# Kernel optimization log

Hardware: AMD Instinct MI355X
Metric: run time of the kernel (lower is better)

## Reference

```python
import math
import jax, jax.numpy as jnp
import numpy as np

D_MODEL = 1024
N_HEADS = 16
BLOCK = 2048
EPS2 = 0.0487        # sparse_eps2 / BOOTSTRAP_EPS2
ROPE_BASE = 10000.0


def _riemann_zeros(K):
    """Approximate imaginary parts of the first K nontrivial zeta zeros by
    Newton-inverting t/(2pi)*log(t/(2pi*e)) = n - 7/8 (standard asymptotic).
    Note: gamma is normalized by gamma[0] in the module, so only the relative
    spacing matters for the math."""
    n = np.arange(1, K + 1, dtype=np.float64)
    t = 10.0 + 6.0 * n  # safe init, > 2*pi
    for _ in range(60):
        f = t / (2 * np.pi) * np.log(t / (2 * np.pi * np.e)) - (n - 0.875)
        fp = np.log(t / (2 * np.pi)) / (2 * np.pi)
        t = t - f / fp
    return t


def _constants(N, K):
    g = _riemann_zeros(K)
    g = g / g[0]
    denom = 0.25 + g * g
    w_re = (0.5 / denom).astype(np.float32)          # [K]
    w_im = (-g / denom).astype(np.float32)           # [K]
    pos = np.arange(N, dtype=np.float32)
    k_idx = np.arange(K, dtype=np.float32)
    inv_freq = ROPE_BASE ** (-k_idx / K)
    phase = pos[:, None] * inv_freq[None, :]          # [N,K]
    cos_p = np.cos(phase).astype(np.float32)
    sin_p = np.sin(phase).astype(np.float32)
    log1p = np.log1p(pos)
    log_decay = (0.5 * (log1p[None, :] - log1p[:, None])).astype(np.float32)  # [N,N]
    tril = np.tril(np.ones((N, N), dtype=bool))
    return (jnp.asarray(w_re), jnp.asarray(w_im), jnp.asarray(cos_p),
            jnp.asarray(sin_p), jnp.asarray(log_decay), jnp.asarray(tril))


def setup_inputs() -> dict:
    key = jax.random.key(0)
    kx, kq, kk, kv, ko = jax.random.split(key, 5)
    B, N, D = 2, BLOCK, D_MODEL
    s = 0.02
    return {
        "x": jax.random.normal(kx, (B, N, D), jnp.float32),
        "Wq": jax.random.normal(kq, (D, D), jnp.float32) * s,
        "Wk": jax.random.normal(kk, (D, D), jnp.float32) * s,
        "Wv": jax.random.normal(kv, (D, D), jnp.float32) * s,
        "Wo": jax.random.normal(ko, (D, D), jnp.float32) * s,
    }


def reference(x, Wq, Wk, Wv, Wo):
    B, N, D = x.shape
    H = N_HEADS
    dh = D // H
    K = dh // 2
    w_re, w_im, cos_p, sin_p, log_decay, tril = _constants(N, K)

    q = (x @ Wq).reshape(B, N, H, dh)
    k = (x @ Wk).reshape(B, N, H, dh)
    v = (x @ Wv).reshape(B, N, H, dh)

    q_re, q_im = q[..., 0::2], q[..., 1::2]           # [B,N,H,K]
    k_re, k_im = k[..., 0::2], k[..., 1::2]

    cos_b = cos_p[None, :, None, :]                   # [1,N,1,K]
    sin_b = sin_p[None, :, None, :]
    # RoPE rotation in complex form
    qt_re = cos_b * q_re + sin_b * q_im
    qt_im = cos_b * q_im - sin_b * q_re
    kt_re = cos_b * k_re + sin_b * k_im
    kt_im = cos_b * k_im - sin_b * k_re

    wr = w_re[None, None, None, :]
    wi = w_im[None, None, None, :]
    # zeta-amplitude complex weighting of q
    qh_re = wr * qt_re - wi * qt_im
    qh_im = wr * qt_im + wi * qt_re

    # Re(sum_k w_k * q~_i conj(k~_j)) via two real GEMMs
    scores = (jnp.einsum('bihk,bjhk->bhij', qh_re, kt_re)
              + jnp.einsum('bihk,bjhk->bhij', qh_im, kt_im)) / math.sqrt(dh)

    # decay_mode == 'mult'
    scores = scores * jnp.exp(log_decay)[None, None, :, :]

    scores = jnp.where(tril[None, None, :, :], scores, -jnp.inf)
    attn = jax.nn.softmax(scores, axis=-1)

    # bootstrap_sparse: keep top-k per row, renormalize
    kk = max(1, math.ceil(EPS2 * N))
    if kk < N:
        vals, _ = jax.lax.top_k(attn, kk)
        thresh = vals[..., -1:]
        mask = (attn >= thresh).astype(attn.dtype)
        masked = attn * mask
        attn = masked / jnp.maximum(masked.sum(-1, keepdims=True), 1e-9)

    out = jnp.einsum('bhij,bjhd->bihd', attn, v).reshape(B, N, D)
    return out @ Wo
```

## Files before the change

### kernel.cpp

```cpp
#include <hip/hip_runtime.h>
#include <math.h>

#define B_SZ 2
#define N_SEQ 2048
#define DM 1024
#define H_HEADS 16
#define DH 64
#define KC 32
#define TOPK 100
#define TQ 16
#define KT 128
#define NTMAX 16
#define FCAP 192

typedef _Float16 half2_t __attribute__((ext_vector_type(2)));
typedef _Float16 half4_t __attribute__((ext_vector_type(4)));
typedef _Float16 half8_t __attribute__((ext_vector_type(8)));
typedef float floatx4 __attribute__((ext_vector_type(4)));
typedef unsigned short ushort4_t __attribute__((ext_vector_type(4)));

__device__ __forceinline__ unsigned short h2us(_Float16 h) {
  unsigned short u; __builtin_memcpy(&u, &h, 2); return u;
}
__device__ __forceinline__ _Float16 us2h(unsigned short u) {
  _Float16 h; __builtin_memcpy(&h, &u, 2); return h;
}
__device__ __forceinline__ unsigned okey16(unsigned short us) {
  return (us & 0x8000u) ? (unsigned)(unsigned short)~us
                        : (unsigned)(us | 0x8000u);
}

__device__ __forceinline__ void stage16(const _Float16* g, _Float16* lds_base,
                                        int lane) {
#if __has_builtin(__builtin_amdgcn_global_load_lds)
  __builtin_amdgcn_global_load_lds(
      (const __attribute__((address_space(1))) void*)g,
      (__attribute__((address_space(3))) void*)lds_base, 16, 0, 0);
#else
  *(half8_t*)(lds_base + lane * 8) = *(const half8_t*)g;
#endif
}

__global__ void const_kernel(float* __restrict__ wre, float* __restrict__ wim) {
  __shared__ double g0s;
  const int k = threadIdx.x;
  const double PI = 3.14159265358979323846;
  const double E_ = 2.71828182845904523536;
  double n = (double)(k + 1);
  double t = 10.0 + 6.0 * n;
  for (int it = 0; it < 60; ++it) {
    double f  = t / (2.0 * PI) * log(t / (2.0 * PI * E_)) - (n - 0.875);
    double fp = log(t / (2.0 * PI)) / (2.0 * PI);
    t = t - f / fp;
  }
  if (k == 0) g0s = t;
  __syncthreads();
  double g = t / g0s;
  double denom = 0.25 + g * g;
  wre[k] = (float)(0.5 / denom);
  wim[k] = (float)(-g / denom);
}

__global__ __launch_bounds__(256) void rope_kernel(float* __restrict__ cosT,
                                                   float* __restrict__ sinT) {
  int idx = blockIdx.x * 256 + threadIdx.x;
  int kk = idx & 31, n = idx >> 5;
  double inv_freq = pow(10000.0, -(double)kk / 32.0);
  double ph = (double)n * inv_freq;
  cosT[idx] = (float)cos(ph);
  sinT[idx] = (float)sin(ph);
}

__global__ __launch_bounds__(256) void cast_x(const float* __restrict__ x,
                                              _Float16* __restrict__ xh) {
  int idx = blockIdx.x * 256 + threadIdx.x;
  float4 v = ((const float4*)x)[idx];
  half4_t h;
  h[0] = (_Float16)v.x; h[1] = (_Float16)v.y;
  h[2] = (_Float16)v.z; h[3] = (_Float16)v.w;
  ((half4_t*)xh)[idx] = h;
}

__global__ __launch_bounds__(256) void transpose_cast(
    const float* __restrict__ W0, const float* __restrict__ W1,
    const float* __restrict__ W2, const float* __restrict__ W3,
    _Float16* __restrict__ T0, _Float16* __restrict__ T1,
    _Float16* __restrict__ T2, _Float16* __restrict__ T3) {
  __shared__ float t[64][65];
  const float* W; _Float16* T;
  switch (blockIdx.z) {
    case 0: W = W0; T = T0; break;
    case 1: W = W1; T = T1; break;
    case 2: W = W2; T = T2; break;
    default: W = W3; T = T3; break;
  }
  const int bx = blockIdx.x;
  const int by = blockIdx.y;
  const int tid = threadIdx.x;
  const int c = tid & 15, rr = tid >> 4;
#pragma unroll
  for (int i = 0; i < 4; ++i) {
    int k = rr + i * 16;
    float4 v = *(const float4*)(W + (size_t)(bx * 64 + k) * DM + by * 64 + c * 4);
    t[k][c * 4 + 0] = v.x; t[k][c * 4 + 1] = v.y;
    t[k][c * 4 + 2] = v.z; t[k][c * 4 + 3] = v.w;
  }
  __syncthreads();
#pragma unroll
  for (int i = 0; i < 4; ++i) {
    int n = rr + i * 16;
    half4_t h;
    h[0] = (_Float16)t[c * 4 + 0][n];
    h[1] = (_Float16)t[c * 4 + 1][n];
    h[2] = (_Float16)t[c * 4 + 2][n];
    h[3] = (_Float16)t[c * 4 + 3][n];
    *(half4_t*)(T + (size_t)(by * 64 + n) * DM + bx * 64 + c * 4) = h;
  }
}

template <typename OutT>
__device__ __forceinline__ void gemm_mfma_body(const _Float16* __restrict__ A,
                                               const _Float16* __restrict__ Bt,
                                               OutT* __restrict__ C) {
  __shared__ _Float16 As[128 * 32];
  __shared__ _Float16 Bs[128 * 32];
  const int tid = threadIdx.x;
  const int wave = tid >> 6, lane = tid & 63;
  const int wm = wave >> 1, wn = wave & 1;
  const int bm = blockIdx.x * 128, bn = blockIdx.y * 128;
  const int lrow = lane >> 2;
  const int lkb = (lane & 3) * 8;
  const int l16 = lane & 15, lq = lane >> 4;
  floatx4 acc[4][4] = {};

  for (int k0 = 0; k0 < DM; k0 += 32) {
    __syncthreads();
#pragma unroll
    for (int s2 = 0; s2 < 2; ++s2) {
      const int seg = wave * 2 + s2;
      stage16(A + (size_t)(bm + seg * 16 + lrow) * DM + k0 + lkb,
              As + seg * 512, lane);
      stage16(Bt + (size_t)(bn + seg * 16 + lrow) * DM + k0 + lkb,
              Bs + seg * 512, lane);
    }
    __syncthreads();
    half8_t af[4], bf[4];
#pragma unroll
    for (int mi = 0; mi < 4; ++mi)
      af[mi] = *(const half8_t*)(As + (wm * 64 + mi * 16 + l16) * 32 + lq * 8);
#pragma unroll
    for (int ni = 0; ni < 4; ++ni)
      bf[ni] = *(const half8_t*)(Bs + (wn * 64 + ni * 16 + l16) * 32 + lq * 8);
#pragma unroll
    for (int mi = 0; mi < 4; ++mi)
#pragma unroll
      for (int ni = 0; ni < 4; ++ni)
        acc[mi][ni] = __builtin_amdgcn_mfma_f32_16x16x32_f16(
            af[mi], bf[ni], acc[mi][ni], 0, 0, 0);
  }
#pragma unroll
  for (int mi = 0; mi < 4; ++mi)
#pragma unroll
    for (int ni = 0; ni < 4; ++ni) {
      const int col = bn + wn * 64 + ni * 16 + l16;
#pragma unroll
      for (int r = 0; r < 4; ++r) {
        const int row = bm + wm * 64 + mi * 16 + lq * 4 + r;
        C[(size_t)row * DM + col] = (OutT)acc[mi][ni][r];
      }
    }
}

__global__ __launch_bounds__(256) void gemm_qkv_mfma(
    const _Float16* __restrict__ xh, const _Float16* __restrict__ Wt0,
    const _Float16* __restrict__ Wt1, const _Float16* __restrict__ Wt2,
    _Float16* __restrict__ q, _Float16* __restrict__ k,
    _Float16* __restrict__ v) {
  const _Float16* Bt; _Float16* C;
  if (blockIdx.z == 0)      { Bt = Wt0; C = q; }
  else if (blockIdx.z == 1) { Bt = Wt1; C = k; }
  else                      { Bt = Wt2; C = v; }
  gemm_mfma_body<_Float16>(xh, Bt, C);
}

__global__ __launch_bounds__(256) void gemm_out_mfma(
    const _Float16* __restrict__ A, const _Float16* __restrict__ Bt,
    float* __restrict__ C) {
  gemm_mfma_body<float>(A, Bt, C);
}

__global__ __launch_bounds__(256) void transform_kernel(
    const _Float16* __restrict__ q, const _Float16* __restrict__ k,
    const _Float16* __restrict__ v, const float* __restrict__ wre,
    const float* __restrict__ wim, const float* __restrict__ cosT,
    const float* __restrict__ sinT, float* __restrict__ qh,
    _Float16* __restrict__ kth, _Float16* __restrict__ vth) {
  int idx = blockIdx.x * blockDim.x + threadIdx.x;
  int kk = idx & 31;
  int h  = (idx >> 5) & 15;
  int n  = (idx >> 9) & 2047;
  int b  = idx >> 20;

  size_t base_in = ((size_t)(b * N_SEQ + n)) * DM + h * DH;
  float q_re = (float)q[base_in + 2 * kk], q_im = (float)q[base_in + 2 * kk + 1];
  float k_re = (float)k[base_in + 2 * kk], k_im = (float)k[base_in + 2 * kk + 1];

  float cp = cosT[n * 32 + kk], sp = sinT[n * 32 + kk];

  float qt_re = cp * q_re + sp * q_im;
  float qt_im = cp * q_im - sp * q_re;
  float ktr   = cp * k_re + sp * k_im;
  float kti   = cp * k_im - sp * k_re;

  float wr = wre[kk], wi = wim[kk];
  float qh_re = wr * qt_re - wi * qt_im;
  float qh_im = wr * qt_im + wi * qt_re;

  float sj = 0.125f * sqrtf(1.0f + (float)n);

  size_t base_out = ((size_t)((b * H_HEADS + h) * N_SEQ + n)) * DH;
  qh[base_out + kk]      = qh_re;
  qh[base_out + 32 + kk] = qh_im;
  kth[base_out + kk]      = (_Float16)(ktr * sj);
  kth[base_out + 32 + kk] = (_Float16)(kti * sj);
  vth[base_out + 2 * kk]     = v[base_in + 2 * kk];
  vth[base_out + 2 * kk + 1] = v[base_in + 2 * kk + 1];
}

__global__ __launch_bounds__(512, 4) void attn_kernel(
    const float* __restrict__ qh, const _Float16* __restrict__ kth,
    const _Float16* __restrict__ vth, _Float16* __restrict__ oh) {
  __shared__ __align__(16) _Float16 ktile[KT][76];
  __shared__ unsigned hist[TQ][128];
  __shared__ unsigned final_[TQ][FCAP];
  __shared__ float mredw[8][TQ];
  __shared__ float rowm[TQ], rowsum[TQ];
  __shared__ unsigned cnt2[TQ], tkA[TQ];
  __shared__ int sh_b[TQ], sh_k[TQ];

  const int tile = gridDim.x - 1 - blockIdx.x;
  const int bh   = blockIdx.y;
  const int i0   = tile * TQ;
  const int tid  = threadIdx.x;
  const int wv = tid >> 6, lane = tid & 63;
  const int l16 = lane & 15, lq = lane >> 4;
  const int jbase = wv * 16 + l16;

  const _Float16* kbase = kth + (size_t)bh * N_SEQ * DH;
  const _Float16* vbase = vth + (size_t)bh * N_SEQ * DH;

#pragma unroll
  for (int u = 0; u < 4; ++u) ((unsigned*)hist)[u * 512 + tid] = 0;
  if (tid < TQ) { cnt2[tid] = 0; rowsum[tid] = 0.f; }

  half8_t af0, af1;
  {
    const float* qrow = qh + ((size_t)(bh * N_SEQ + i0 + l16)) * DH;
    const float rs = rsqrtf(1.0f + (float)(i0 + l16));
    float4 a0 = *(const float4*)(qrow + lq * 8);
    float4 a1 = *(const float4*)(qrow + lq * 8 + 4);
    float4 b0 = *(const float4*)(qrow + 32 + lq * 8);
    float4 b1 = *(const float4*)(qrow + 32 + lq * 8 + 4);
    af0[0] = (_Float16)(a0.x * rs); af0[1] = (_Float16)(a0.y * rs);
    af0[2] = (_Float16)(a0.z * rs); af0[3] = (_Float16)(a0.w * rs);
    af0[4] = (_Float16)(a1.x * rs); af0[5] = (_Float16)(a1.y * rs);
    af0[6] = (_Float16)(a1.z * rs); af0[7] = (_Float16)(a1.w * rs);
    af1[0] = (_Float16)(b0.x * rs); af1[1] = (_Float16)(b0.y * rs);
    af1[2] = (_Float16)(b0.z * rs); af1[3] = (_Float16)(b0.w * rs);
    af1[4] = (_Float16)(b1.x * rs); af1[5] = (_Float16)(b1.y * rs);
    af1[6] = (_Float16)(b1.z * rs); af1[7] = (_Float16)(b1.w * rs);
  }

  const int ntile = (i0 + TQ + KT - 1) / KT;

  ushort4_t scr[NTMAX];
  float mx[4] = {-INFINITY, -INFINITY, -INFINITY, -INFINITY};

#pragma unroll
  for (int t = 0; t < NTMAX; ++t) {
    if (t < ntile) {
      const int j0 = t * KT;
      __syncthreads();
#pragma unroll
      for (int u = 0; u < 2; ++u) {
        int idx = u * 512 + tid;
        int row = idx >> 3, c8 = idx & 7;
        *(half8_t*)&ktile[row][c8 * 8] =
            *(const half8_t*)(kbase + (size_t)(j0 + row) * DH + c8 * 8);
      }
      __syncthreads();
      half8_t bf0 = *(const half8_t*)&ktile[jbase][lq * 8];
      half8_t bf1 = *(const half8_t*)&ktile[jbase][32 + lq * 8];
      floatx4 acc = {};
      acc = __builtin_amdgcn_mfma_f32_16x16x32_f16(af0, bf0, acc, 0, 0, 0);
      acc = __builtin_amdgcn_mfma_f32_16x16x32_f16(af1, bf1, acc, 0, 0, 0);
      const int jc = j0 + jbase;
      ushort4_t s4;
#pragma unroll
      for (int r = 0; r < 4; ++r) {
        float sc = acc[r];
        s4[r] = h2us((_Float16)sc);
        if (jc <= i0 + lq * 4 + r) {
          mx[r] = fmaxf(mx[r], sc);
          unsigned hb = okey16(s4[r]) >> 8;
          atomicAdd(&hist[lq * 4 + r][hb >> 1], 1u << ((hb & 1) * 16));
        }
      }
      scr[t] = s4;
    }
  }

#pragma unroll
  for (int g = 1; g <= 8; g <<= 1)
#pragma unroll
    for (int r = 0; r < 4; ++r) mx[r] = fmaxf(mx[r], __shfl_xor(mx[r], g));
  if (l16 == 0)
#pragma unroll
    for (int r = 0; r < 4; ++r) mredw[wv][lq * 4 + r] = mx[r];
  __syncthreads();
  if (tid < TQ) {
    float m = mredw[0][tid];
#pragma unroll
    for (int w = 1; w < 8; ++w) m = fmaxf(m, mredw[w][tid]);
    rowm[tid] = m;
  }

  const int srow = tid >> 5, ts = tid & 31;
  {
    const int L = i0 + srow + 1;
    if (L > TOPK) {
      const unsigned* hrow = hist[srow];
      const int base_u = 124 - 4 * ts;
      unsigned h0 = hrow[base_u + 0], h1 = hrow[base_u + 1];
      unsigned h2 = hrow[base_u + 2], h3 = hrow[base_u + 3];
      int c[8] = {(int)(h3 >> 16), (int)(h3 & 0xffffu),
                  (int)(h2 >> 16), (int)(h2 & 0xffffu),
                  (int)(h1 >> 16), (int)(h1 & 0xffffu),
                  (int)(h0 >> 16), (int)(h0 & 0xffffu)};
      int ssum = 0;
#pragma unroll
      for (int k2 = 0; k2 < 8; ++k2) ssum += c[k2];
      int inc = ssum;
#pragma unroll
      for (int d = 1; d < 32; d <<= 1) {
        int o = __shfl_up(inc, d, 32);
        if (ts >= d) inc += o;
      }
      const int excl = inc - ssum;
      if (excl < TOPK && TOPK <= inc) {
        int cum = excl, k2 = 0;
#pragma unroll
        for (; k2 < 8; ++k2) {
          if (cum + c[k2] >= TOPK) break;
          cum += c[k2];
        }
        sh_b[srow] = 255 - 8 * ts - k2;
        sh_k[srow] = TOPK - cum;
      }
    } else if (ts == 0) {
      sh_b[srow] = 256;
      sh_k[srow] = 0;
      tkA[srow] = 0;
    }
  }
  __syncthreads();
#pragma unroll
  for (int u = 0; u < 4; ++u) ((unsigned*)hist)[u * 512 + tid] = 0;
  int bh4[4];
#pragma unroll
  for (int r = 0; r < 4; ++r) bh4[r] = sh_b[lq * 4 + r];
  __syncthreads();

#pragma unroll
  for (int t = 0; t < NTMAX; ++t) {
    if (t < ntile) {
      const int jc = t * KT + jbase;
      ushort4_t s4 = scr[t];
#pragma unroll
      for (int r = 0; r < 4; ++r) {
        if (jc <= i0 + lq * 4 + r) {
          unsigned key = okey16(s4[r]);
          if ((int)(key >> 8) == bh4[r]) {
            unsigned lb = key & 255u;
            atomicAdd(&hist[lq * 4 + r][lb >> 1], 1u << ((lb & 1) * 16));
          }
        }
      }
    }
  }
  __syncthreads();

  {
    const int L = i0 + srow + 1;
    if (L > TOPK) {
      const int krem = sh_k[srow];
      const unsigned* hrow = hist[srow];
      const int base_u = 124 - 4 * ts;
      unsigned h0 = hrow[base_u + 0], h1 = hrow[base_u + 1];
      unsigned h2 = hrow[base_u + 2], h3 = hrow[base_u + 3];
      int c[8] = {(int)(h3 >> 16), (int)(h3 & 0xffffu),
                  (int)(h2 >> 16), (int)(h2 & 0xffffu),
                  (int)(h1 >> 16), (int)(h1 & 0xffffu),
                  (int)(h0 >> 16), (int)(h0 & 0xffffu)};
      int ssum = 0;
#pragma unroll
      for (int k2 = 0; k2 < 8; ++k2) ssum += c[k2];
      int inc = ssum;
#pragma unroll
      for (int d = 1; d < 32; d <<= 1) {
        int o = __shfl_up(inc, d, 32);
        if (ts >= d) inc += o;
      }
      const int excl = inc - ssum;
      if (excl < krem && krem <= inc) {
        int cum = excl, k2 = 0;
#pragma unroll
        for (; k2 < 8; ++k2) {
          if (cum + c[k2] >= krem) break;
          cum += c[k2];
        }
        tkA[srow] = ((unsigned)sh_b[srow] << 8) | (unsigned)(255 - 8 * ts - k2);
      }
    }
  }
  __syncthreads();

  unsigned tk4[4]; float m4[4];
#pragma unroll
  for (int r = 0; r < 4; ++r) {
    tk4[r] = tkA[lq * 4 + r];
    m4[r]  = rowm[lq * 4 + r];
  }
  float lsum[4] = {0.f, 0.f, 0.f, 0.f};
#pragma unroll
  for (int t = 0; t < NTMAX; ++t) {
    if (t < ntile) {
      const int jc = t * KT + jbase;
      ushort4_t s4 = scr[t];
#pragma unroll
      for (int r = 0; r < 4; ++r) {
        if (jc <= i0 + lq * 4 + r) {
          unsigned short us = s4[r];
          if (okey16(us) >= tk4[r]) {
            float p = expf((float)us2h(us) - m4[r]);
            lsum[r] += p;
            unsigned pos = atomicAdd(&cnt2[lq * 4 + r], 1u);
            if (pos < FCAP)
              final_[lq * 4 + r][pos] =
                  ((unsigned)h2us((_Float16)p) << 16) | (unsigned)jc;
          }
        }
      }
    }
  }
#pragma unroll
  for (int g = 1; g <= 8; g <<= 1)
#pragma unroll
    for (int r = 0; r < 4; ++r) lsum[r] += __shfl_xor(lsum[r], g);
  if (l16 == 0)
#pragma unroll
    for (int r = 0; r < 4; ++r) atomicAdd(&rowsum[lq * 4 + r], lsum[r]);
  __syncthreads();

  for (int rr = wv; rr < TQ; rr += 8) {
    const int nfin = (int)min(cnt2[rr], (unsigned)FCAP);
    const float inv = 1.0f / rowsum[rr];
    float acc = 0.f;
#pragma unroll 4
    for (int s = 0; s < nfin; ++s) {
      unsigned e = final_[rr][s];
      const int jj = (int)(e & 0xffffu);
      const float p = (float)us2h((unsigned short)(e >> 16));
      acc += p * (float)vbase[(size_t)jj * DH + lane];
    }
    const int b = bh >> 4, h = bh & 15;
    const int i = i0 + rr;
    oh[((size_t)(b * N_SEQ + i)) * DM + h * DH + lane] = (_Float16)(acc * inv);
  }
}

extern "C" void kernel_launch(void* const* d_in, const int* in_sizes, int n_in,
                              void* d_out, int out_size, void* d_ws, size_t ws_size,
                              hipStream_t stream) {
  const float* x  = (const float*)d_in[0];
  const float* Wq = (const float*)d_in[1];
  const float* Wk = (const float*)d_in[2];
  const float* Wv = (const float*)d_in[3];
  const float* Wo = (const float*)d_in[4];
  float* out = (float*)d_out;
  char* ws = (char*)d_ws;

  const size_t MAT = (size_t)B_SZ * N_SEQ * DM;
  const size_t WSZ = (size_t)DM * DM;

  float*    qh   = (float*)ws;                       ws += MAT * 4;
  _Float16* xh   = (_Float16*)ws;                    ws += MAT * 2;
  _Float16* qf   = (_Float16*)ws;                    ws += MAT * 2;
  _Float16* kf   = (_Float16*)ws;                    ws += MAT * 2;
  _Float16* vf   = (_Float16*)ws;                    ws += MAT * 2;
  _Float16* kth  = (_Float16*)ws;                    ws += MAT * 2;
  _Float16* vth  = (_Float16*)ws;                    ws += MAT * 2;
  _Float16* Wt0  = (_Float16*)ws;                    ws += WSZ * 2;
  _Float16* Wt1  = (_Float16*)ws;                    ws += WSZ * 2;
  _Float16* Wt2  = (_Float16*)ws;                    ws += WSZ * 2;
  _Float16* Wt3  = (_Float16*)ws;                    ws += WSZ * 2;
  float*    wre  = (float*)ws;                       ws += KC * 4;
  float*    wim  = (float*)ws;                       ws += KC * 4;
  float*    cosT = (float*)ws;                       ws += (size_t)N_SEQ * KC * 4;
  float*    sinT = (float*)ws;                       ws += (size_t)N_SEQ * KC * 4;
  _Float16* oh   = xh;

  const_kernel<<<1, 32, 0, stream>>>(wre, wim);
  rope_kernel<<<(N_SEQ * KC) / 256, 256, 0, stream>>>(cosT, sinT);
  cast_x<<<(int)(MAT / 4 / 256), 256, 0, stream>>>(x, xh);
  transpose_cast<<<dim3(16, 16, 4), 256, 0, stream>>>(Wq, Wk, Wv, Wo,
                                                      Wt0, Wt1, Wt2, Wt3);
  gemm_qkv_mfma<<<dim3(32, 8, 3), 256, 0, stream>>>(xh, Wt0, Wt1, Wt2,
                                                    qf, kf, vf);
  transform_kernel<<<(B_SZ * N_SEQ * H_HEADS * KC) / 256, 256, 0, stream>>>(
      qf, kf, vf, wre, wim, cosT, sinT, qh, kth, vth);
  attn_kernel<<<dim3(N_SEQ / TQ, B_SZ * H_HEADS), 512, 0, stream>>>(
      qh, kth, vth, oh);
  gemm_out_mfma<<<dim3(32, 8, 1), 256, 0, stream>>>(oh, Wt3, out);
}
```

Measured before the change: 427.8 us.

## Prefetch next K tile into registers and keep score cache in named registers

```diff
diff --git a/kernel.cpp b/kernel.cpp
--- a/kernel.cpp
+++ b/kernel.cpp
@@ -227,6 +227,9 @@
   vth[base_out + 2 * kk + 1] = v[base_in + 2 * kk + 1];
 }
 
+#define REPEAT16(M) M(0) M(1) M(2) M(3) M(4) M(5) M(6) M(7) \
+                    M(8) M(9) M(10) M(11) M(12) M(13) M(14) M(15)
+
 __global__ __launch_bounds__(512, 4) void attn_kernel(
     const float* __restrict__ qh, const _Float16* __restrict__ kth,
     const _Float16* __restrict__ vth, _Float16* __restrict__ oh) {
@@ -248,6 +251,11 @@
 
   const _Float16* kbase = kth + (size_t)bh * N_SEQ * DH;
   const _Float16* vbase = vth + (size_t)bh * N_SEQ * DH;
+
+  const int row0 = tid >> 3, c80 = tid & 7;
+  const int row1 = 64 + row0;
+  const _Float16* gk0 = kbase + (size_t)row0 * DH + c80 * 8;
+  const _Float16* gk1 = kbase + (size_t)row1 * DH + c80 * 8;
 
 #pragma unroll
   for (int u = 0; u < 4; ++u) ((unsigned*)hist)[u * 512 + tid] = 0;
@@ -273,42 +281,45 @@
 
   const int ntile = (i0 + TQ + KT - 1) / KT;
 
-  ushort4_t scr[NTMAX];
+  ushort4_t scr0{}, scr1{}, scr2{}, scr3{}, scr4{}, scr5{}, scr6{}, scr7{},
+      scr8{}, scr9{}, scr10{}, scr11{}, scr12{}, scr13{}, scr14{}, scr15{};
   float mx[4] = {-INFINITY, -INFINITY, -INFINITY, -INFINITY};
 
-#pragma unroll
-  for (int t = 0; t < NTMAX; ++t) {
-    if (t < ntile) {
-      const int j0 = t * KT;
-      __syncthreads();
-#pragma unroll
-      for (int u = 0; u < 2; ++u) {
-        int idx = u * 512 + tid;
-        int row = idx >> 3, c8 = idx & 7;
-        *(half8_t*)&ktile[row][c8 * 8] =
-            *(const half8_t*)(kbase + (size_t)(j0 + row) * DH + c8 * 8);
-      }
-      __syncthreads();
-      half8_t bf0 = *(const half8_t*)&ktile[jbase][lq * 8];
-      half8_t bf1 = *(const half8_t*)&ktile[jbase][32 + lq * 8];
-      floatx4 acc = {};
-      acc = __builtin_amdgcn_mfma_f32_16x16x32_f16(af0, bf0, acc, 0, 0, 0);
-      acc = __builtin_amdgcn_mfma_f32_16x16x32_f16(af1, bf1, acc, 0, 0, 0);
-      const int jc = j0 + jbase;
-      ushort4_t s4;
-#pragma unroll
-      for (int r = 0; r < 4; ++r) {
-        float sc = acc[r];
-        s4[r] = h2us((_Float16)sc);
-        if (jc <= i0 + lq * 4 + r) {
-          mx[r] = fmaxf(mx[r], sc);
-          unsigned hb = okey16(s4[r]) >> 8;
-          atomicAdd(&hist[lq * 4 + r][hb >> 1], 1u << ((hb & 1) * 16));
-        }
-      }
-      scr[t] = s4;
-    }
-  }
+  half8_t rA = *(const half8_t*)gk0;
+  half8_t rB = *(const half8_t*)gk1;
+
+#define PASS_A(T)                                                             \
+  if ((T) < ntile) {                                                          \
+    const int j0 = (T) * KT;                                                  \
+    __syncthreads();                       \
+    *(half8_t*)&ktile[row0][c80 * 8] = rA;                                    \
+    *(half8_t*)&ktile[row1][c80 * 8] = rB;                                    \
+    __syncthreads();                                     \
+    if ((T) + 1 < ntile) {                                                    \
+      rA = *(const half8_t*)(gk0 + (size_t)(j0 + KT) * DH);                   \
+      rB = *(const half8_t*)(gk1 + (size_t)(j0 + KT) * DH);                   \
+    }                                                                         \
+    half8_t bf0 = *(const half8_t*)&ktile[jbase][lq * 8];                     \
+    half8_t bf1 = *(const half8_t*)&ktile[jbase][32 + lq * 8];                \
+    floatx4 acc = {};                                                         \
+    acc = __builtin_amdgcn_mfma_f32_16x16x32_f16(af0, bf0, acc, 0, 0, 0);     \
+    acc = __builtin_amdgcn_mfma_f32_16x16x32_f16(af1, bf1, acc, 0, 0, 0);     \
+    const int jc = j0 + jbase;                                                \
+    ushort4_t s4;                                                             \
+    _Pragma("unroll")                                                         \
+    for (int r = 0; r < 4; ++r) {                                             \
+      float sc = acc[r];                                                      \
+      s4[r] = h2us((_Float16)sc);                                             \
+      if (jc <= i0 + lq * 4 + r) {                                            \
+        mx[r] = fmaxf(mx[r], sc);                                             \
+        unsigned hb = okey16(s4[r]) >> 8;                                     \
+        atomicAdd(&hist[lq * 4 + r][hb >> 1], 1u << ((hb & 1) * 16));         \
+      }                                                                       \
+    }                                                                         \
+    scr##T = s4;                                                              \
+  }
+  REPEAT16(PASS_A)
+#undef PASS_A
 
 #pragma unroll
   for (int g = 1; g <= 8; g <<= 1)
@@ -371,23 +382,22 @@
   for (int r = 0; r < 4; ++r) bh4[r] = sh_b[lq * 4 + r];
   __syncthreads();
 
-#pragma unroll
-  for (int t = 0; t < NTMAX; ++t) {
-    if (t < ntile) {
-      const int jc = t * KT + jbase;
-      ushort4_t s4 = scr[t];
-#pragma unroll
-      for (int r = 0; r < 4; ++r) {
-        if (jc <= i0 + lq * 4 + r) {
-          unsigned key = okey16(s4[r]);
-          if ((int)(key >> 8) == bh4[r]) {
-            unsigned lb = key & 255u;
-            atomicAdd(&hist[lq * 4 + r][lb >> 1], 1u << ((lb & 1) * 16));
-          }
-        }
-      }
-    }
-  }
+#define PASS_B(T)                                                             \
+  if ((T) < ntile) {                                                          \
+    const int jc = (T) * KT + jbase;                                          \
+    _Pragma("unroll")                                                         \
+    for (int r = 0; r < 4; ++r) {                                             \
+      if (jc <= i0 + lq * 4 + r) {                                            \
+        unsigned key = okey16(scr##T[r]);                                     \
+        if ((int)(key >> 8) == bh4[r]) {                                      \
+          unsigned lb = key & 255u;                                           \
+          atomicAdd(&hist[lq * 4 + r][lb >> 1], 1u << ((lb & 1) * 16));       \
+        }                                                                     \
+      }                                                                       \
+    }                                                                         \
+  }
+  REPEAT16(PASS_B)
+#undef PASS_B
   __syncthreads();
 
   {
@@ -432,27 +442,26 @@
     m4[r]  = rowm[lq * 4 + r];
   }
   float lsum[4] = {0.f, 0.f, 0.f, 0.f};
-#pragma unroll
-  for (int t = 0; t < NTMAX; ++t) {
-    if (t < ntile) {
-      const int jc = t * KT + jbase;
-      ushort4_t s4 = scr[t];
-#pragma unroll
-      for (int r = 0; r < 4; ++r) {
-        if (jc <= i0 + lq * 4 + r) {
-          unsigned short us = s4[r];
-          if (okey16(us) >= tk4[r]) {
-            float p = expf((float)us2h(us) - m4[r]);
-            lsum[r] += p;
-            unsigned pos = atomicAdd(&cnt2[lq * 4 + r], 1u);
-            if (pos < FCAP)
-              final_[lq * 4 + r][pos] =
-                  ((unsigned)h2us((_Float16)p) << 16) | (unsigned)jc;
-          }
-        }
-      }
-    }
-  }
+#define PASS_C(T)                                                             \
+  if ((T) < ntile) {                                                          \
+    const int jc = (T) * KT + jbase;                                          \
+    _Pragma("unroll")                                                         \
+    for (int r = 0; r < 4; ++r) {                                             \
+      if (jc <= i0 + lq * 4 + r) {                                            \
+        unsigned short us = scr##T[r];                                        \
+        if (okey16(us) >= tk4[r]) {                                           \
+          float p = __expf((float)us2h(us) - m4[r]);                          \
+          lsum[r] += p;                                                       \
+          unsigned pos = atomicAdd(&cnt2[lq * 4 + r], 1u);                    \
+          if (pos < FCAP)                                                     \
+            final_[lq * 4 + r][pos] =                                         \
+                ((unsigned)h2us((_Float16)p) << 16) | (unsigned)jc;           \
+        }                                                                     \
+      }                                                                       \
+    }                                                                         \
+  }
+  REPEAT16(PASS_C)
+#undef PASS_C
 #pragma unroll
   for (int g = 1; g <= 8; g <<= 1)
 #pragma unroll
@@ -462,20 +471,32 @@
     for (int r = 0; r < 4; ++r) atomicAdd(&rowsum[lq * 4 + r], lsum[r]);
   __syncthreads();
 
-  for (int rr = wv; rr < TQ; rr += 8) {
-    const int nfin = (int)min(cnt2[rr], (unsigned)FCAP);
-    const float inv = 1.0f / rowsum[rr];
-    float acc = 0.f;
+  {
+    const int r0 = wv, r1 = wv + 8;
+    const int n0 = (int)min(cnt2[r0], (unsigned)FCAP);
+    const int n1 = (int)min(cnt2[r1], (unsigned)FCAP);
+    const float inv0 = 1.0f / rowsum[r0];
+    const float inv1 = 1.0f / rowsum[r1];
+    float a0 = 0.f, a1 = 0.f;
+    const int nmx = n0 > n1 ? n0 : n1;
 #pragma unroll 4
-    for (int s = 0; s < nfin; ++s) {
-      unsigned e = final_[rr][s];
-      const int jj = (int)(e & 0xffffu);
-      const float p = (float)us2h((unsigned short)(e >> 16));
-      acc += p * (float)vbase[(size_t)jj * DH + lane];
+    for (int s = 0; s < nmx; ++s) {
+      if (s < n0) {
+        unsigned e = final_[r0][s];
+        a0 += (float)us2h((unsigned short)(e >> 16)) *
+              (float)vbase[(size_t)(e & 0xffffu) * DH + lane];
+      }
+      if (s < n1) {
+        unsigned e = final_[r1][s];
+        a1 += (float)us2h((unsigned short)(e >> 16)) *
+              (float)vbase[(size_t)(e & 0xffffu) * DH + lane];
+      }
     }
     const int b = bh >> 4, h = bh & 15;
-    const int i = i0 + rr;
-    oh[((size_t)(b * N_SEQ + i)) * DM + h * DH + lane] = (_Float16)(acc * inv);
+    oh[((size_t)(b * N_SEQ + i0 + r0)) * DM + h * DH + lane] =
+        (_Float16)(a0 * inv0);
+    oh[((size_t)(b * N_SEQ + i0 + r1)) * DM + h * DH + lane] =
+        (_Float16)(a1 * inv1);
   }
 }
 
```

Measured after the change: 586.7 us. 37.1% more time.

## Deepen GEMM K-tile to 64 with XOR-swizzled LDS and cheaper constant kernels

Applied to the files above, without the earlier changes.

```diff
diff --git a/kernel.cpp b/kernel.cpp
--- a/kernel.cpp
+++ b/kernel.cpp
@@ -48,7 +48,7 @@
   const double E_ = 2.71828182845904523536;
   double n = (double)(k + 1);
   double t = 10.0 + 6.0 * n;
-  for (int it = 0; it < 60; ++it) {
+  for (int it = 0; it < 16; ++it) {
     double f  = t / (2.0 * PI) * log(t / (2.0 * PI * E_)) - (n - 0.875);
     double fp = log(t / (2.0 * PI)) / (2.0 * PI);
     t = t - f / fp;
@@ -65,10 +65,11 @@
                                                    float* __restrict__ sinT) {
   int idx = blockIdx.x * 256 + threadIdx.x;
   int kk = idx & 31, n = idx >> 5;
-  double inv_freq = pow(10000.0, -(double)kk / 32.0);
-  double ph = (double)n * inv_freq;
-  cosT[idx] = (float)cos(ph);
-  sinT[idx] = (float)sin(ph);
+  float f = -(float)kk * (13.2877123795494f / 32.0f);
+  float inv_freq = exp2f(f);
+  float ph = (float)n * inv_freq;
+  cosT[idx] = cosf(ph);
+  sinT[idx] = sinf(ph);
 }
 
 __global__ __launch_bounds__(256) void cast_x(const float* __restrict__ x,
@@ -122,41 +123,49 @@
 __device__ __forceinline__ void gemm_mfma_body(const _Float16* __restrict__ A,
                                                const _Float16* __restrict__ Bt,
                                                OutT* __restrict__ C) {
-  __shared__ _Float16 As[128 * 32];
-  __shared__ _Float16 Bs[128 * 32];
+  __shared__ _Float16 As[128 * 64];
+  __shared__ _Float16 Bs[128 * 64];
   const int tid = threadIdx.x;
   const int wave = tid >> 6, lane = tid & 63;
   const int wm = wave >> 1, wn = wave & 1;
   const int bm = blockIdx.x * 128, bn = blockIdx.y * 128;
-  const int lrow = lane >> 2;
-  const int lkb = (lane & 3) * 8;
+  const int grow = lane >> 3;
+  const int gch  = (lane & 7) ^ grow;
   const int l16 = lane & 15, lq = lane >> 4;
+  const int sw  = l16 & 7;
   floatx4 acc[4][4] = {};
 
-  for (int k0 = 0; k0 < DM; k0 += 32) {
+  for (int k0 = 0; k0 < DM; k0 += 64) {
     __syncthreads();
 #pragma unroll
-    for (int s2 = 0; s2 < 2; ++s2) {
-      const int seg = wave * 2 + s2;
-      stage16(A + (size_t)(bm + seg * 16 + lrow) * DM + k0 + lkb,
+    for (int s = 0; s < 4; ++s) {
+      const int seg = wave * 4 + s;
+      stage16(A + (size_t)(bm + seg * 8 + grow) * DM + k0 + gch * 8,
               As + seg * 512, lane);
-      stage16(Bt + (size_t)(bn + seg * 16 + lrow) * DM + k0 + lkb,
+      stage16(Bt + (size_t)(bn + seg * 8 + grow) * DM + k0 + gch * 8,
               Bs + seg * 512, lane);
     }
     __syncthreads();
-    half8_t af[4], bf[4];
-#pragma unroll
-    for (int mi = 0; mi < 4; ++mi)
-      af[mi] = *(const half8_t*)(As + (wm * 64 + mi * 16 + l16) * 32 + lq * 8);
-#pragma unroll
-    for (int ni = 0; ni < 4; ++ni)
-      bf[ni] = *(const half8_t*)(Bs + (wn * 64 + ni * 16 + l16) * 32 + lq * 8);
-#pragma unroll
-    for (int mi = 0; mi < 4; ++mi)
+    half8_t af[2][4], bf[2][4];
+#pragma unroll
+    for (int kk2 = 0; kk2 < 2; ++kk2) {
+#pragma unroll
+      for (int mi = 0; mi < 4; ++mi)
+        af[kk2][mi] = *(const half8_t*)(As + (wm * 64 + mi * 16 + l16) * 64 +
+                                        ((kk2 * 4 + lq) ^ sw) * 8);
 #pragma unroll
       for (int ni = 0; ni < 4; ++ni)
-        acc[mi][ni] = __builtin_amdgcn_mfma_f32_16x16x32_f16(
-            af[mi], bf[ni], acc[mi][ni], 0, 0, 0);
+        bf[kk2][ni] = *(const half8_t*)(Bs + (wn * 64 + ni * 16 + l16) * 64 +
+                                        ((kk2 * 4 + lq) ^ sw) * 8);
+    }
+#pragma unroll
+    for (int kk2 = 0; kk2 < 2; ++kk2)
+#pragma unroll
+      for (int mi = 0; mi < 4; ++mi)
+#pragma unroll
+        for (int ni = 0; ni < 4; ++ni)
+          acc[mi][ni] = __builtin_amdgcn_mfma_f32_16x16x32_f16(
+              af[kk2][mi], bf[kk2][ni], acc[mi][ni], 0, 0, 0);
   }
 #pragma unroll
   for (int mi = 0; mi < 4; ++mi)
```

Result: faster. 410.3 us (-4.1%).
